# Kernel tuning notes

Measured on AMD Instinct MI355X. Metric: run time of the kernel, lower is better.

Reference implementation:

```python
import jax, jax.numpy as jnp
import numpy as np

BATCH, L = 2, 1024
D_MODEL, D_INNER, D_STATE, DT_RANK, K = 2048, 4096, 16, 128, 4


def setup_inputs() -> dict:
    key = jax.random.key(0)
    ks = jax.random.split(key, 9)
    g = lambda i, shape, s: jax.random.normal(ks[i], shape, jnp.float32) * s
    A_log = jnp.log(jnp.broadcast_to(jnp.arange(1, D_STATE + 1, dtype=jnp.float32),
                                     (D_INNER, D_STATE)))
    return {
        "hidden_states": g(0, (BATCH, L, D_MODEL), 1.0),
        "W_in": g(1, (2 * D_INNER, D_MODEL), 0.02),
        "conv_w": g(2, (D_INNER, K), 0.2),
        "conv_b": g(3, (D_INNER,), 0.02),
        "W_x": g(4, (DT_RANK + 2 * D_STATE, D_INNER), 0.02),
        "W_dt": g(5, (D_INNER, DT_RANK), 0.02),
        "b_dt": g(6, (D_INNER,), 0.02),
        "A_log": A_log,
        "D": jnp.ones((D_INNER,), jnp.float32),
        "W_out": g(7, (D_MODEL, D_INNER), 0.02),
        "b_out": g(8, (D_MODEL,), 0.02),
    }


def reference(hidden_states, W_in, conv_w, conv_b, W_x, W_dt, b_dt, A_log, D, W_out, b_out):
    b, l, _ = hidden_states.shape
    # in_proj -> (b, 2*d_inner, l), split into x and gate z
    xz = jnp.einsum('bld,ed->bel', hidden_states, W_in)
    x, z = jnp.split(xz, 2, axis=1)                      # each (b, d_inner, l)
    # conv_state = F.pad(x, (d_conv - l, 0)): keeps the last d_conv timesteps
    conv_state = x[:, :, -K:]
    # causal depthwise conv1d (left pad K-1) + SiLU
    xc = jax.lax.conv_general_dilated(
        x, conv_w[:, None, :], window_strides=(1,), padding=[(K - 1, 0)],
        feature_group_count=D_INNER, dimension_numbers=('NCH', 'OIH', 'NCH'))
    xc = jax.nn.silu(xc + conv_b[None, :, None])         # (b, d_inner, l)
    # x_proj -> dt / B / C
    x_dbl = jnp.einsum('bdl,ed->ble', xc, W_x)           # (b, l, dt_rank+2n)
    dt, Bm, Cm = jnp.split(x_dbl, [DT_RANK, DT_RANK + D_STATE], axis=-1)
    dt = jnp.einsum('blr,dr->bdl', dt, W_dt)             # (b, d_inner, l), no bias here
    delta = jax.nn.softplus(dt + b_dt[None, :, None])    # dt_proj bias folded into softplus
    A = -jnp.exp(A_log)                                  # (d_inner, d_state)

    def step(state, inp):                                # state: (b, d_inner, d_state)
        d_t, b_t, c_t, u_t = inp                         # (b,d), (b,n), (b,n), (b,d)
        dA = jnp.exp(d_t[..., None] * A)                 # (b, d, n)
        state = dA * state + (d_t * u_t)[..., None] * b_t[:, None, :]
        y_t = jnp.einsum('bdn,bn->bd', state, c_t)
        return state, y_t

    xs = (delta.transpose(2, 0, 1),                      # (l, b, d)
          Bm.transpose(1, 0, 2),                         # (l, b, n)
          Cm.transpose(1, 0, 2),
          xc.transpose(2, 0, 1))
    init = jnp.zeros((b, D_INNER, D_STATE), delta.dtype)
    last_state, ys = jax.lax.scan(step, init, xs)
    y = ys.transpose(1, 2, 0) + D[None, :, None] * xc    # (b, d_inner, l) skip term
    y = y * jax.nn.silu(z)                               # gating
    out = jnp.einsum('bdl,ed->ble', y, W_out) + b_out    # (b, l, d_model)
    return out, conv_state, last_state
```

## Files before the change

kernel.cpp:

```cpp
#include <hip/hip_runtime.h>
#include <stdint.h>
#include <stddef.h>

typedef __bf16 bf16;
typedef __attribute__((ext_vector_type(2))) __bf16 bf16x2;
typedef __attribute__((ext_vector_type(4))) __bf16 bf16x4;
typedef __attribute__((ext_vector_type(8))) __bf16 bf16x8;
typedef __attribute__((ext_vector_type(4))) float floatx4;

#define GAS __attribute__((address_space(1)))
#define LAS __attribute__((address_space(3)))

__device__ __forceinline__ void async16(const void* g, void* l) {
  __builtin_amdgcn_global_load_lds((const GAS void*)g, (LAS void*)l, 16, 0, 0);
}

__device__ __forceinline__ bf16x8 cvt8(const float* p) {
  floatx4 a = *(const floatx4*)p;
  floatx4 b = *(const floatx4*)(p + 4);
  bf16x8 r;
  r[0] = (bf16)a[0]; r[1] = (bf16)a[1]; r[2] = (bf16)a[2]; r[3] = (bf16)a[3];
  r[4] = (bf16)b[0]; r[5] = (bf16)b[1]; r[6] = (bf16)b[2]; r[7] = (bf16)b[3];
  return r;
}

#define ENGINE_BODY(K0_EXPR, NT_EXPR, EPILOGUE)                                \
  __shared__ __attribute__((aligned(16))) bf16 SA[2][2][8192];                 \
  __shared__ __attribute__((aligned(16))) bf16 SB[2][2][8192];                 \
  const int tid = threadIdx.x;                                                 \
  const int wave = tid >> 6;                                                   \
  const int lane = tid & 63;                                                   \
  const int lr = lane & 15;                                                    \
  const int kg = lane >> 4;                                                    \
  const int wm = (wave >> 2) * 128;                                            \
  const int wn = (wave & 3) * 64;                                              \
  const int tilesM = M >> 8;                                                   \
  const int tm = blockIdx.x % tilesM;                                          \
  const int tn = blockIdx.x / tilesM;                                          \
  const int rowBase = tm * 256;                                                \
  const int colBase = tn * 256;                                                \
  const int k0 = (K0_EXPR);                                                    \
  const int NT = (NT_EXPR);                                                    \
  const int srow = tid >> 2;                                                   \
  const int ske = (tid & 3) << 3;                                              \
  const int skel = ske ^ (((srow >> 1) & 3) << 3);                             \
  const size_t aRow0 = (size_t)(rowBase + srow) * lda;                         \
  const size_t aRow1 = aRow0 + (size_t)128 * lda;                              \
  const size_t bRow0 = (size_t)(colBase + srow) * ldb;                         \
  const size_t bRow1 = bRow0 + (size_t)128 * ldb;                              \
  const int keSh = (kg << 3) ^ (((lr >> 1) & 3) << 3);                         \
  floatx4 acc[8][4] = {};                                                      \
  bf16x8 af0[4], af1[4], bgA[4], bgB[4];                                       \
  auto stA = [&](int buf, int kh, int kt) {                                    \
    const int gk = k0 + kt * 64 + kh * 32 + skel;                              \
    bf16* d = &SA[buf][kh][0];                                                 \
    async16(A + aRow0 + gk, d + tid * 8);                                      \
    async16(A + aRow1 + gk, d + 4096 + tid * 8);                               \
  };                                                                           \
  auto stB = [&](int buf, int kh, int kt) {                                    \
    const int gk = k0 + kt * 64 + kh * 32 + skel;                              \
    bf16* d = &SB[buf][kh][0];                                                 \
    async16(B + bRow0 + gk, d + tid * 8);                                      \
    async16(B + bRow1 + gk, d + 4096 + tid * 8);                               \
  };                                                                           \
  stB(0, 0, 0); stA(0, 0, 0); stB(0, 1, 0); stA(0, 1, 0);                      \
  stB(1, 0, 1); stA(1, 0, 1); stB(1, 1, 1);                                    \
  asm volatile("s_waitcnt vmcnt(0)" ::: "memory");                             \
  __builtin_amdgcn_s_barrier();                                                \
  RD_B(bgA, 0, 0);                                                             \
  RD_A(af0, 0, 0, 0);                                                          \
  for (int it = 0; it < (NT >> 1); ++it) {                                     \
    const int T0 = it * 2;                                                     \
    const int T1 = T0 + 1;                                                     \
    const int s1 = (T0 + 2 < NT) ? T0 + 2 : NT - 1;                            \
    const int s2 = (T1 + 2 < NT) ? T1 + 2 : NT - 1;                            \
    PH(RD_A(af1, 0, 0, 1), 4, stA(1, 1, T1), bgA, af0, 0, false)               \
    PH(RD_B(bgB, 0, 1); RD_A(af0, 0, 1, 0), 8, stB(0, 0, s1), bgA, af1, 1,     \
       false)                                                                  \
    PH(RD_A(af1, 0, 1, 1), 4, stA(0, 0, s1), bgB, af0, 0, false)               \
    PH(RD_B(bgA, 1, 0); RD_A(af0, 1, 0, 0), 8, stB(0, 1, s1), bgB, af1, 1,     \
       true)                                                                   \
    PH(RD_A(af1, 1, 0, 1), 4, stA(0, 1, s1), bgA, af0, 0, false)               \
    PH(RD_B(bgB, 1, 1); RD_A(af0, 1, 1, 0), 8, stB(1, 0, s2), bgA, af1, 1,     \
       false)                                                                  \
    PH(RD_A(af1, 1, 1, 1), 4, stA(1, 0, s2), bgB, af0, 0, false)               \
    PH(RD_B(bgA, 0, 0); RD_A(af0, 0, 0, 0), 8, stB(1, 1, s2), bgB, af1, 1,     \
       true)                                                                   \
  }                                                                            \
  asm volatile("s_waitcnt vmcnt(0) lgkmcnt(0)" ::: "memory");                  \
  _Pragma("unroll") for (int m = 0; m < 8; ++m) {                              \
    _Pragma("unroll") for (int n = 0; n < 4; ++n) {                            \
      const int col = colBase + wn + n * 16 + lr;                              \
      _Pragma("unroll") for (int r = 0; r < 4; ++r) {                          \
        const int row = rowBase + wm + m * 16 + kg * 4 + r;                    \
        const size_t idx = (size_t)row * N + col;                              \
        EPILOGUE;                                                              \
      }                                                                        \
    }                                                                          \
  }

#define RD_B(DST, BUF, KH)                                                     \
  _Pragma("unroll") for (int n = 0; n < 4; ++n)                                \
      DST[n] = *(const bf16x8*)&SB[BUF][KH][(wn + n * 16 + lr) * 32 + keSh];
#define RD_A(DST, BUF, KH, MH)                                                 \
  _Pragma("unroll") for (int m = 0; m < 4; ++m)                                \
      DST[m] =                                                                 \
          *(const bf16x8*)&SA[BUF][KH][(wm + ((MH)*4 + m) * 16 + lr) * 32 +    \
                                       keSh];
#define PH(RDS, CNT, STG, BGR, AFR, MH, VM)                                    \
  {                                                                            \
    RDS;                                                                       \
    STG;                                                                       \
    __builtin_amdgcn_s_barrier();                                              \
    asm volatile("s_waitcnt lgkmcnt(" #CNT ")" ::: "memory");                  \
    __builtin_amdgcn_sched_barrier(0);                                         \
    __builtin_amdgcn_s_setprio(1);                                             \
    _Pragma("unroll") for (int m = 0; m < 4; ++m)                              \
      _Pragma("unroll") for (int n = 0; n < 4; ++n)                            \
          acc[(MH)*4 + m][n] = __builtin_amdgcn_mfma_f32_16x16x32_bf16(        \
              AFR[m], BGR[n], acc[(MH)*4 + m][n], 0, 0, 0);                    \
    __builtin_amdgcn_s_setprio(0);                                             \
    __builtin_amdgcn_sched_barrier(0);                                         \
    if constexpr (VM) asm volatile("s_waitcnt vmcnt(2)" ::: "memory");         \
    __builtin_amdgcn_s_barrier();                                              \
  }

__global__ __launch_bounds__(512, 2) void gemm256_8p(
    const bf16* __restrict__ A, const bf16* __restrict__ B,
    bf16* __restrict__ C, int M, int N, int K, int lda, int ldb) {
  ENGINE_BODY(0, K >> 6, C[idx] = (bf16)acc[m][n][r])
}

__global__ __launch_bounds__(512, 2) void gemm256_sk(
    const bf16* __restrict__ A, const bf16* __restrict__ B,
    bf16* __restrict__ C, int M, int N, int K, int lda, int ldb) {
  ENGINE_BODY(blockIdx.y * (K / gridDim.y), (K / gridDim.y) >> 6,
              C[(size_t)blockIdx.y * 4194304 + idx] = (bf16)acc[m][n][r])
}
#undef PH
#undef RD_A
#undef RD_B
#undef ENGINE_BODY

template <int EPI, int AF, int BF, int TM>
__global__ __launch_bounds__(256, 4) void gemm_bt(
    const void* __restrict__ Aptr, const void* __restrict__ Bptr,
    void* __restrict__ Cout, const float* __restrict__ bias,
    int M, int N, int K, int lda, int ldb) {
  __shared__ bf16 As[TM * 32];
  __shared__ bf16 Bs[128 * 32];
  const int tid = threadIdx.x;

  int bx = blockIdx.x, by = blockIdx.y;
  if constexpr (EPI == 6) {
    const int f = blockIdx.x + gridDim.x * blockIdx.y;
    const int gy = gridDim.y >> 3;
    const int i = f >> 3;
    by = (f & 7) * gy + (i % gy);
    bx = i / gy;
  }
  const int rowBase = bx * TM;
  const int colBase = by * 128;
  const int kLen = K / gridDim.z;
  const int k0 = blockIdx.z * kLen;
  const int kIters = kLen / 32;

  const int sRow = tid >> 2;
  const int sCol = (tid & 3) << 3;
  const int wave = tid >> 6;
  const int lane = tid & 63;
  constexpr int MI = 4;
  constexpr int NJ = (TM == 128) ? 4 : 2;
  const int wm = (TM == 128) ? ((wave >> 1) << 6) : 0;
  const int wn = (TM == 128) ? ((wave & 1) << 6) : (wave << 5);
  const int lr = lane & 15;
  const int kg = lane >> 4;

  floatx4 acc[MI][NJ] = {};

  for (int kt = 0; kt < kIters; ++kt) {
    const int kk = k0 + kt * 32;
    __syncthreads();
    if constexpr (AF) {
      const float* pa =
          (const float*)Aptr + (size_t)(rowBase + sRow) * lda + kk + sCol;
      *(bf16x8*)&As[tid * 8] = cvt8(pa);
      if constexpr (TM == 128)
        *(bf16x8*)&As[2048 + tid * 8] = cvt8(pa + (size_t)64 * lda);
    } else {
      const bf16* pa =
          (const bf16*)Aptr + (size_t)(rowBase + sRow) * lda + kk + sCol;
      async16(pa, &As[tid * 8]);
      if constexpr (TM == 128)
        async16(pa + (size_t)64 * lda, &As[2048 + tid * 8]);
    }
    if constexpr (BF) {
      const float* pb =
          (const float*)Bptr + (size_t)(colBase + sRow) * ldb + kk + sCol;
      *(bf16x8*)&Bs[tid * 8] = cvt8(pb);
      *(bf16x8*)&Bs[2048 + tid * 8] = cvt8(pb + (size_t)64 * ldb);
    } else {
      const bf16* pb =
          (const bf16*)Bptr + (size_t)(colBase + sRow) * ldb + kk + sCol;
      async16(pb, &Bs[tid * 8]);
      async16(pb + (size_t)64 * ldb, &Bs[2048 + tid * 8]);
    }
    __syncthreads();

    bf16x8 af[MI], bg[NJ];
#pragma unroll
    for (int i = 0; i < MI; ++i)
      af[i] = *(const bf16x8*)&As[(wm + i * 16 + lr) * 32 + kg * 8];
#pragma unroll
    for (int j = 0; j < NJ; ++j)
      bg[j] = *(const bf16x8*)&Bs[(wn + j * 16 + lr) * 32 + kg * 8];
#pragma unroll
    for (int i = 0; i < MI; ++i)
#pragma unroll
      for (int j = 0; j < NJ; ++j)
        acc[i][j] = __builtin_amdgcn_mfma_f32_16x16x32_bf16(af[i], bg[j],
                                                            acc[i][j], 0, 0, 0);
  }

#pragma unroll
  for (int i = 0; i < MI; ++i) {
#pragma unroll
    for (int j = 0; j < NJ; ++j) {
      const int col = colBase + wn + j * 16 + lr;
      float bv = 0.f;
      if constexpr (EPI == 2 || EPI == 3) bv = bias[col];
#pragma unroll
      for (int r = 0; r < 4; ++r) {
        const int row = rowBase + wm + i * 16 + kg * 4 + r;
        const size_t idx = (size_t)row * N + col;
        float v = acc[i][j][r];
        if constexpr (EPI == 0) {
          ((bf16*)Cout)[idx] = (bf16)v;
        } else if constexpr (EPI == 1) {
          atomicAdd((float*)Cout + idx, v);
        } else if constexpr (EPI == 2) {
          v += bv;
          const float t = __expf(v);
          const float sp = (v > 20.f) ? v : __logf(1.f + t);
          ((bf16*)Cout)[idx] = (bf16)sp;
        } else if constexpr (EPI == 3) {
          ((float*)Cout)[idx] = v + bv;
        } else if constexpr (EPI == 4) {
          ((float*)Cout)[(size_t)blockIdx.z * 524288 + idx] = v;
        } else {
          ((bf16*)Cout)[(size_t)blockIdx.z * 4194304 + idx] = (bf16)v;
        }
      }
    }
  }
}

__global__ __launch_bounds__(256) void reduce_xdbl(
    const float* __restrict__ part, float* __restrict__ xdbl,
    bf16* __restrict__ xdblb) {
  const size_t i4 = ((size_t)blockIdx.x * 256 + threadIdx.x) * 4;
  floatx4 s = {};
#pragma unroll
  for (int z = 0; z < 8; ++z) {
    const floatx4 v = *(const floatx4*)&part[(size_t)z * 524288 + i4];
    s[0] += v[0]; s[1] += v[1]; s[2] += v[2]; s[3] += v[3];
  }
  *(floatx4*)&xdbl[i4] = s;
  const int col = (int)(i4 & 255);
  if (col < 128) {
    const size_t row = i4 >> 8;
    bf16x4 b;
    b[0] = (bf16)s[0]; b[1] = (bf16)s[1]; b[2] = (bf16)s[2]; b[3] = (bf16)s[3];
    *(bf16x4*)&xdblb[row * 128 + col] = b;
  }
}

__global__ __launch_bounds__(256) void reduce_out4(
    const bf16* __restrict__ part, const float* __restrict__ bias,
    float* __restrict__ outp) {
  const size_t i4 = ((size_t)blockIdx.x * 256 + threadIdx.x) * 4;
  floatx4 s = *(const floatx4*)&bias[i4 & 2047];
#pragma unroll
  for (int z = 0; z < 4; ++z) {
    const bf16x4 v = *(const bf16x4*)&part[(size_t)z * 4194304 + i4];
    s[0] += (float)v[0]; s[1] += (float)v[1];
    s[2] += (float)v[2]; s[3] += (float)v[3];
  }
  *(floatx4*)&outp[i4] = s;
}

#define PC0 524288UL
#define PC1 2621440UL
#define PC2 2686976UL
#define PC3 3735552UL
#define PC4 3866624UL
__global__ __launch_bounds__(256) void prep_all(
    const float* __restrict__ h, const float* __restrict__ wi,
    const float* __restrict__ wd, const float* __restrict__ wo,
    const float* __restrict__ wx, bf16* __restrict__ hb,
    bf16* __restrict__ wib, bf16* __restrict__ wdb, bf16* __restrict__ wob,
    bf16* __restrict__ wxp) {
  const size_t c = (size_t)blockIdx.x * 256 + threadIdx.x;
  if (c < PC0) {
    const size_t e = c * 8;
    *(bf16x8*)&hb[e] = cvt8(&h[e]);
  } else if (c < PC1) {
    const size_t e = (c - PC0) * 8;
    *(bf16x8*)&wib[e] = cvt8(&wi[e]);
  } else if (c < PC2) {
    const size_t e = (c - PC1) * 8;
    *(bf16x8*)&wdb[e] = cvt8(&wd[e]);
  } else if (c < PC3) {
    const size_t e = (c - PC2) * 8;
    *(bf16x8*)&wob[e] = cvt8(&wo[e]);
  } else if (c < PC4) {
    const size_t e = (c - PC3) * 8;
    if ((e >> 12) < 160) {
      *(bf16x8*)&wxp[e] = cvt8(&wx[e]);
    } else {
      bf16x8 z = {};
      *(bf16x8*)&wxp[e] = z;
    }
  }
}

__global__ void wxpad_prep(const float* __restrict__ Wx,
                           bf16* __restrict__ WXPAD) {
  const int idx = blockIdx.x * 256 + threadIdx.x;
  const int row = idx >> 12;
  WXPAD[idx] = (row < 160) ? (bf16)Wx[idx] : (bf16)0.f;
}

__global__ __launch_bounds__(256) void conv_v8(
    const bf16* __restrict__ XZ, const float* __restrict__ conv_w,
    const float* __restrict__ conv_b, bf16* __restrict__ XC,
    float* __restrict__ outConv) {
  const int idx = blockIdx.x * 256 + threadIdx.x;
  const int d8 = (idx & 511) << 3;
  const int row = idx >> 9;
  const int l = row & 1023;
  float acc[8];
  {
    const floatx4 cb0 = *(const floatx4*)&conv_b[d8];
    const floatx4 cb1 = *(const floatx4*)&conv_b[d8 + 4];
#pragma unroll
    for (int j = 0; j < 4; ++j) { acc[j] = cb0[j]; acc[4 + j] = cb1[j]; }
  }
  float w[8][4];
#pragma unroll
  for (int j = 0; j < 8; ++j) {
    const floatx4 cw = *(const floatx4*)&conv_w[(d8 + j) * 4];
#pragma unroll
    for (int k = 0; k < 4; ++k) w[j][k] = cw[k];
  }
  if (l >= 3) {
#pragma unroll
    for (int k = 0; k < 4; ++k) {
      const bf16x8 x = *(const bf16x8*)&XZ[(size_t)(row - 3 + k) * 8192 + d8];
#pragma unroll
      for (int j = 0; j < 8; ++j) acc[j] += w[j][k] * (float)x[j];
    }
  } else {
#pragma unroll
    for (int k = 0; k < 4; ++k) {
      if (l - 3 + k >= 0) {
        const bf16x8 x = *(const bf16x8*)&XZ[(size_t)(row - 3 + k) * 8192 + d8];
#pragma unroll
        for (int j = 0; j < 8; ++j) acc[j] += w[j][k] * (float)x[j];
      }
    }
  }
  bf16x8 o;
#pragma unroll
  for (int j = 0; j < 8; ++j)
    o[j] = (bf16)(acc[j] / (1.f + __expf(-acc[j])));
  *(bf16x8*)&XC[(size_t)row * 4096 + d8] = o;
  if (idx < 4096) {
#pragma unroll
    for (int j = 0; j < 8; ++j) {
      const int e = idx * 8 + j;
      const int k = e & 3;
      const int dd = (e >> 2) & 4095;
      const int b = e >> 14;
      outConv[e] = (float)XZ[(size_t)(b * 1024 + 1020 + k) * 8192 + dd];
    }
  }
}

#define NCH 32
#define CLEN 32
#define LOG2E 1.44269504088896f

__global__ __launch_bounds__(256) void scan_phase1(
    const bf16* __restrict__ DELTA, const bf16* __restrict__ XC,
    const float* __restrict__ XDBL, const float* __restrict__ A_log,
    bf16* __restrict__ P, bf16* __restrict__ Lc) {
  const int pd = blockIdx.x * 256 + threadIdx.x;
  const int c = blockIdx.y;
  const int b = pd >> 11;
  const int d = (pd & 2047) << 1;
  const int bd = (b << 12) + d;
  float A2[32], st[32], p[32];
#pragma unroll
  for (int n = 0; n < 32; ++n) {
    A2[n] = -__expf(A_log[d * 16 + n]) * LOG2E;
    st[n] = 0.f;
    p[n] = 1.f;
  }
  size_t row = (size_t)b * 1024 + (size_t)c * CLEN;
  for (int t = 0; t < CLEN; ++t, ++row) {
    const bf16x2 d2 = *(const bf16x2*)&DELTA[row * 4096 + d];
    const bf16x2 u2 = *(const bf16x2*)&XC[row * 4096 + d];
    const float dlt0 = (float)d2[0], dlt1 = (float)d2[1];
    const float du0 = dlt0 * (float)u2[0], du1 = dlt1 * (float)u2[1];
    const float* __restrict__ Bp = XDBL + row * 256 + 128;
#pragma unroll
    for (int n = 0; n < 16; ++n) {
      const float Bv = Bp[n];
      const float dA0 = exp2f(dlt0 * A2[n]);
      st[n] = dA0 * st[n] + du0 * Bv;
      p[n] *= dA0;
      const float dA1 = exp2f(dlt1 * A2[16 + n]);
      st[16 + n] = dA1 * st[16 + n] + du1 * Bv;
      p[16 + n] *= dA1;
    }
  }
  const size_t o = ((size_t)c * 8192 + bd) * 16;
  bf16x8 pk[4], lk[4];
#pragma unroll
  for (int n = 0; n < 32; ++n) {
    pk[n >> 3][n & 7] = (bf16)p[n];
    lk[n >> 3][n & 7] = (bf16)st[n];
  }
#pragma unroll
  for (int q = 0; q < 4; ++q) {
    *(bf16x8*)&P[o + q * 8] = pk[q];
    *(bf16x8*)&Lc[o + q * 8] = lk[q];
  }
}

__global__ __launch_bounds__(64) void scan_phase2(
    const bf16* __restrict__ P, const bf16* __restrict__ Lc,
    bf16* __restrict__ In, float* __restrict__ lastOut) {
  const int bd = blockIdx.x * 64 + threadIdx.x;
  float st[16] = {};
  for (int c = 0; c < NCH; ++c) {
    const size_t o = ((size_t)c * 8192 + bd) * 16;
    const bf16x8 p0 = *(const bf16x8*)&P[o];
    const bf16x8 p1 = *(const bf16x8*)&P[o + 8];
    const bf16x8 l0 = *(const bf16x8*)&Lc[o];
    const bf16x8 l1 = *(const bf16x8*)&Lc[o + 8];
    bf16x8 w0, w1;
#pragma unroll
    for (int n = 0; n < 8; ++n) {
      w0[n] = (bf16)st[n];
      w1[n] = (bf16)st[8 + n];
    }
    *(bf16x8*)&In[o] = w0;
    *(bf16x8*)&In[o + 8] = w1;
#pragma unroll
    for (int n = 0; n < 8; ++n) {
      st[n] = (float)p0[n] * st[n] + (float)l0[n];
      st[8 + n] = (float)p1[n] * st[8 + n] + (float)l1[n];
    }
  }
  const int b = bd >> 12;
  const int d = bd & 4095;
#pragma unroll
  for (int n = 0; n < 16; ++n)
    lastOut[(size_t)b * 65536 + d * 16 + n] = st[n];
}

__global__ __launch_bounds__(256) void scan_phase3(
    const bf16* __restrict__ DELTA, const bf16* __restrict__ XC,
    const bf16* __restrict__ XZ, const float* __restrict__ XDBL,
    const float* __restrict__ A_log, const float* __restrict__ Dp,
    const bf16* __restrict__ In, bf16* __restrict__ Y) {
  const int pd = blockIdx.x * 256 + threadIdx.x;
  const int c = blockIdx.y;
  const int b = pd >> 11;
  const int d = (pd & 2047) << 1;
  const int bd = (b << 12) + d;
  float A2[32], st[32];
  const size_t o = ((size_t)c * 8192 + bd) * 16;
#pragma unroll
  for (int q = 0; q < 4; ++q) {
    const bf16x8 v = *(const bf16x8*)&In[o + q * 8];
#pragma unroll
    for (int j = 0; j < 8; ++j) st[q * 8 + j] = (float)v[j];
  }
#pragma unroll
  for (int n = 0; n < 32; ++n)
    A2[n] = -__expf(A_log[d * 16 + n]) * LOG2E;
  const float Dd0 = Dp[d], Dd1 = Dp[d + 1];
  size_t row = (size_t)b * 1024 + (size_t)c * CLEN;
  for (int t = 0; t < CLEN; ++t, ++row) {
    const bf16x2 d2 = *(const bf16x2*)&DELTA[row * 4096 + d];
    const bf16x2 u2 = *(const bf16x2*)&XC[row * 4096 + d];
    const bf16x2 z2 = *(const bf16x2*)&XZ[row * 8192 + 4096 + d];
    const float dlt0 = (float)d2[0], dlt1 = (float)d2[1];
    const float u0 = (float)u2[0], u1 = (float)u2[1];
    const float du0 = dlt0 * u0, du1 = dlt1 * u1;
    const float* __restrict__ Bp = XDBL + row * 256 + 128;
    float y0 = 0.f, y1 = 0.f;
#pragma unroll
    for (int n = 0; n < 16; ++n) {
      const float Bv = Bp[n];
      const float Cv = Bp[16 + n];
      const float dA0 = exp2f(dlt0 * A2[n]);
      st[n] = dA0 * st[n] + du0 * Bv;
      y0 += st[n] * Cv;
      const float dA1 = exp2f(dlt1 * A2[16 + n]);
      st[16 + n] = dA1 * st[16 + n] + du1 * Bv;
      y1 += st[16 + n] * Cv;
    }
    const float z0 = (float)z2[0], z1 = (float)z2[1];
    const float sig0 = 1.f / (1.f + __expf(-z0));
    const float sig1 = 1.f / (1.f + __expf(-z1));
    bf16x2 yo;
    yo[0] = (bf16)((y0 + Dd0 * u0) * (z0 * sig0));
    yo[1] = (bf16)((y1 + Dd1 * u1) * (z1 * sig1));
    *(bf16x2*)&Y[row * 4096 + d] = yo;
  }
}

#define OFF_XZ 0UL
#define OFF_XC 33554432UL
#define OFF_DELTA 50331648UL
#define OFF_Y 83886080UL
#define OFF_XDBL 100663296UL
#define OFF_WXPAD 103284736UL
#define OFF_P 105381888UL
#define OFF_L 113770496UL
#define OFF_HBF 122159104UL
#define OFF_WINBF 130547712UL
#define OFF_WDTBF 164102144UL
#define OFF_WOUTBF 165150720UL
#define WS_NEED_CAST 181927936UL

extern "C" void kernel_launch(void* const* d_in, const int* in_sizes, int n_in,
                              void* d_out, int out_size, void* d_ws,
                              size_t ws_size, hipStream_t stream) {
  const float* hidden = (const float*)d_in[0];
  const float* W_in = (const float*)d_in[1];
  const float* conv_w = (const float*)d_in[2];
  const float* conv_b = (const float*)d_in[3];
  const float* W_x = (const float*)d_in[4];
  const float* W_dt = (const float*)d_in[5];
  const float* b_dt = (const float*)d_in[6];
  const float* A_log = (const float*)d_in[7];
  const float* Dvec = (const float*)d_in[8];
  const float* W_out = (const float*)d_in[9];
  const float* b_out = (const float*)d_in[10];

  char* ws = (char*)d_ws;
  bf16* XZ = (bf16*)(ws + OFF_XZ);
  bf16* XC = (bf16*)(ws + OFF_XC);
  bf16* DELTA = (bf16*)(ws + OFF_DELTA);
  float* PART = (float*)(ws + OFF_DELTA + 16777216UL);
  bf16* SLAB3 = (bf16*)(ws + OFF_XZ);
  bf16* Y = (bf16*)(ws + OFF_Y);
  float* XDBL = (float*)(ws + OFF_XDBL);
  bf16* XDBLB = (bf16*)(ws + OFF_HBF);
  bf16* WXPAD = (bf16*)(ws + OFF_WXPAD);
  bf16* P = (bf16*)(ws + OFF_P);
  bf16* Lc = (bf16*)(ws + OFF_L);

  float* out = (float*)d_out;
  float* out_conv = out + 4194304;
  float* out_last = out + 4227072;
  bf16* In = (bf16*)out;

  const bool castOK = ws_size >= WS_NEED_CAST;
  if (castOK) {
    bf16* HBF = (bf16*)(ws + OFF_HBF);
    bf16* WINBF = (bf16*)(ws + OFF_WINBF);
    bf16* WDTBF = (bf16*)(ws + OFF_WDTBF);
    bf16* WOUTBF = (bf16*)(ws + OFF_WOUTBF);
    prep_all<<<15104, 256, 0, stream>>>(hidden, W_in, W_dt, W_out, W_x, HBF,
                                        WINBF, WDTBF, WOUTBF, WXPAD);
    gemm256_8p<<<dim3(256), 512, 0, stream>>>(HBF, WINBF, XZ, 2048, 8192,
                                              2048, 2048, 2048);
    conv_v8<<<4096, 256, 0, stream>>>(XZ, conv_w, conv_b, XC, out_conv);
    gemm_bt<4, 0, 0, 64><<<dim3(32, 2, 8), 256, 0, stream>>>(
        XC, WXPAD, PART, nullptr, 2048, 256, 4096, 4096, 4096);
    reduce_xdbl<<<512, 256, 0, stream>>>(PART, XDBL, XDBLB);
    gemm_bt<2, 0, 0, 64><<<dim3(32, 32, 1), 256, 0, stream>>>(
        XDBLB, WDTBF, DELTA, b_dt, 2048, 4096, 128, 128, 128);
    scan_phase1<<<dim3(16, NCH), 256, 0, stream>>>(DELTA, XC, XDBL, A_log, P,
                                                   Lc);
    scan_phase2<<<128, 64, 0, stream>>>(P, Lc, In, out_last);
    scan_phase3<<<dim3(16, NCH), 256, 0, stream>>>(DELTA, XC, XZ, XDBL, A_log,
                                                   Dvec, In, Y);
    gemm256_sk<<<dim3(64, 4), 512, 0, stream>>>(Y, WOUTBF, SLAB3, 2048, 2048,
                                                4096, 4096, 4096);
    reduce_out4<<<4096, 256, 0, stream>>>(SLAB3, b_out, out);
  } else {
    wxpad_prep<<<4096, 256, 0, stream>>>(W_x, WXPAD);
    gemm_bt<0, 1, 1, 128><<<dim3(16, 64, 1), 256, 0, stream>>>(
        hidden, W_in, XZ, nullptr, 2048, 8192, 2048, 2048, 2048);
    conv_v8<<<4096, 256, 0, stream>>>(XZ, conv_w, conv_b, XC, out_conv);
    gemm_bt<4, 0, 0, 64><<<dim3(32, 2, 8), 256, 0, stream>>>(
        XC, WXPAD, PART, nullptr, 2048, 256, 4096, 4096, 4096);
    reduce_xdbl<<<512, 256, 0, stream>>>(PART, XDBL, XDBLB);
    gemm_bt<2, 1, 1, 64><<<dim3(32, 32, 1), 256, 0, stream>>>(
        XDBL, W_dt, DELTA, b_dt, 2048, 4096, 128, 256, 128);
    scan_phase1<<<dim3(16, NCH), 256, 0, stream>>>(DELTA, XC, XDBL, A_log, P,
                                                   Lc);
    scan_phase2<<<128, 64, 0, stream>>>(P, Lc, In, out_last);
    scan_phase3<<<dim3(16, NCH), 256, 0, stream>>>(DELTA, XC, XZ, XDBL, A_log,
                                                   Dvec, In, Y);
    gemm_bt<6, 0, 1, 128><<<dim3(16, 16, 4), 256, 0, stream>>>(
        Y, W_out, SLAB3, nullptr, 2048, 2048, 4096, 4096, 4096);
    reduce_out4<<<4096, 256, 0, stream>>>(SLAB3, b_out, out);
  }
}
```

Measured before the change: 443.5 us.

## Fuse three scan phases into one cooperative kernel with grid syncs

Replaces the three separate chunked-scan launches (chunk-local scan, cross-chunk carry propagation, final recompute with output gating) with a single cooperative kernel that uses grid-wide syncs between phases. The goal is to remove two kernel launch boundaries and to keep the A coefficients in registers across phases. In exchange, the grid is fixed at 256 blocks of 512 threads with launch_bounds forcing one block per CU. Phase 2 runs on only 128 blocks of 64 threads while the rest of the grid idles at the barrier. If the cooperative launch fails, the code falls back to the original three kernels.

```diff
diff --git a/kernel.cpp b/kernel.cpp
--- a/kernel.cpp
+++ b/kernel.cpp
@@ -1,6 +1,9 @@
 #include <hip/hip_runtime.h>
+#include <hip/hip_cooperative_groups.h>
 #include <stdint.h>
 #include <stddef.h>
+
+namespace cg = cooperative_groups;
 
 typedef __bf16 bf16;
 typedef __attribute__((ext_vector_type(2))) __bf16 bf16x2;
@@ -524,6 +527,139 @@
   }
 }
 
+__global__ __launch_bounds__(512, 1) void scan_fused(
+    const bf16* __restrict__ DELTA, const bf16* __restrict__ XC,
+    const bf16* __restrict__ XZ, const float* __restrict__ XDBL,
+    const float* __restrict__ A_log, const float* __restrict__ Dp,
+    bf16* __restrict__ P, bf16* __restrict__ Lc, bf16* __restrict__ In,
+    float* __restrict__ lastOut, bf16* __restrict__ Y) {
+  cg::grid_group grid = cg::this_grid();
+  const int blk = blockIdx.x;
+  const int tid = threadIdx.x;
+  const int pd = (blk & 7) * 512 + tid;
+  const int c = blk >> 3;
+  const int b = pd >> 11;
+  const int d = (pd & 2047) << 1;
+  const int bd = (b << 12) + d;
+  const size_t o = ((size_t)c * 8192 + bd) * 16;
+
+  float A2[32];
+#pragma unroll
+  for (int n = 0; n < 32; ++n)
+    A2[n] = -__expf(A_log[d * 16 + n]) * LOG2E;
+
+  {
+    float st[32], p[32];
+#pragma unroll
+    for (int n = 0; n < 32; ++n) { st[n] = 0.f; p[n] = 1.f; }
+    size_t row = (size_t)b * 1024 + (size_t)c * CLEN;
+    for (int t = 0; t < CLEN; ++t, ++row) {
+      const bf16x2 d2 = *(const bf16x2*)&DELTA[row * 4096 + d];
+      const bf16x2 u2 = *(const bf16x2*)&XC[row * 4096 + d];
+      const float dlt0 = (float)d2[0], dlt1 = (float)d2[1];
+      const float du0 = dlt0 * (float)u2[0], du1 = dlt1 * (float)u2[1];
+      const float* __restrict__ Bp = XDBL + row * 256 + 128;
+#pragma unroll
+      for (int n = 0; n < 16; ++n) {
+        const float Bv = Bp[n];
+        const float dA0 = exp2f(dlt0 * A2[n]);
+        st[n] = dA0 * st[n] + du0 * Bv;
+        p[n] *= dA0;
+        const float dA1 = exp2f(dlt1 * A2[16 + n]);
+        st[16 + n] = dA1 * st[16 + n] + du1 * Bv;
+        p[16 + n] *= dA1;
+      }
+    }
+    bf16x8 pk[4], lk[4];
+#pragma unroll
+    for (int n = 0; n < 32; ++n) {
+      pk[n >> 3][n & 7] = (bf16)p[n];
+      lk[n >> 3][n & 7] = (bf16)st[n];
+    }
+#pragma unroll
+    for (int q = 0; q < 4; ++q) {
+      *(bf16x8*)&P[o + q * 8] = pk[q];
+      *(bf16x8*)&Lc[o + q * 8] = lk[q];
+    }
+  }
+  __threadfence();
+  grid.sync();
+  __threadfence();
+
+  if (blk < 128 && tid < 64) {
+    const int bd2 = blk * 64 + tid;
+    float st[16] = {};
+    for (int cc = 0; cc < NCH; ++cc) {
+      const size_t o2 = ((size_t)cc * 8192 + bd2) * 16;
+      const bf16x8 p0 = *(const bf16x8*)&P[o2];
+      const bf16x8 p1 = *(const bf16x8*)&P[o2 + 8];
+      const bf16x8 l0 = *(const bf16x8*)&Lc[o2];
+      const bf16x8 l1 = *(const bf16x8*)&Lc[o2 + 8];
+      bf16x8 w0, w1;
+#pragma unroll
+      for (int n = 0; n < 8; ++n) {
+        w0[n] = (bf16)st[n];
+        w1[n] = (bf16)st[8 + n];
+      }
+      *(bf16x8*)&In[o2] = w0;
+      *(bf16x8*)&In[o2 + 8] = w1;
+#pragma unroll
+      for (int n = 0; n < 8; ++n) {
+        st[n] = (float)p0[n] * st[n] + (float)l0[n];
+        st[8 + n] = (float)p1[n] * st[8 + n] + (float)l1[n];
+      }
+    }
+    const int b2 = bd2 >> 12;
+    const int d2i = bd2 & 4095;
+#pragma unroll
+    for (int n = 0; n < 16; ++n)
+      lastOut[(size_t)b2 * 65536 + d2i * 16 + n] = st[n];
+  }
+  __threadfence();
+  grid.sync();
+  __threadfence();
+
+  {
+    float st[32];
+#pragma unroll
+    for (int q = 0; q < 4; ++q) {
+      const bf16x8 v = *(const bf16x8*)&In[o + q * 8];
+#pragma unroll
+      for (int j = 0; j < 8; ++j) st[q * 8 + j] = (float)v[j];
+    }
+    const float Dd0 = Dp[d], Dd1 = Dp[d + 1];
+    size_t row = (size_t)b * 1024 + (size_t)c * CLEN;
+    for (int t = 0; t < CLEN; ++t, ++row) {
+      const bf16x2 d2 = *(const bf16x2*)&DELTA[row * 4096 + d];
+      const bf16x2 u2 = *(const bf16x2*)&XC[row * 4096 + d];
+      const bf16x2 z2 = *(const bf16x2*)&XZ[row * 8192 + 4096 + d];
+      const float dlt0 = (float)d2[0], dlt1 = (float)d2[1];
+      const float u0 = (float)u2[0], u1 = (float)u2[1];
+      const float du0 = dlt0 * u0, du1 = dlt1 * u1;
+      const float* __restrict__ Bp = XDBL + row * 256 + 128;
+      float y0 = 0.f, y1 = 0.f;
+#pragma unroll
+      for (int n = 0; n < 16; ++n) {
+        const float Bv = Bp[n];
+        const float Cv = Bp[16 + n];
+        const float dA0 = exp2f(dlt0 * A2[n]);
+        st[n] = dA0 * st[n] + du0 * Bv;
+        y0 += st[n] * Cv;
+        const float dA1 = exp2f(dlt1 * A2[16 + n]);
+        st[16 + n] = dA1 * st[16 + n] + du1 * Bv;
+        y1 += st[16 + n] * Cv;
+      }
+      const float z0 = (float)z2[0], z1 = (float)z2[1];
+      const float sig0 = 1.f / (1.f + __expf(-z0));
+      const float sig1 = 1.f / (1.f + __expf(-z1));
+      bf16x2 yo;
+      yo[0] = (bf16)((y0 + Dd0 * u0) * (z0 * sig0));
+      yo[1] = (bf16)((y1 + Dd1 * u1) * (z1 * sig1));
+      *(bf16x2*)&Y[row * 4096 + d] = yo;
+    }
+  }
+}
+
 #define OFF_XZ 0UL
 #define OFF_XC 33554432UL
 #define OFF_DELTA 50331648UL
@@ -587,11 +723,23 @@
     reduce_xdbl<<<512, 256, 0, stream>>>(PART, XDBL, XDBLB);
     gemm_bt<2, 0, 0, 64><<<dim3(32, 32, 1), 256, 0, stream>>>(
         XDBLB, WDTBF, DELTA, b_dt, 2048, 4096, 128, 128, 128);
-    scan_phase1<<<dim3(16, NCH), 256, 0, stream>>>(DELTA, XC, XDBL, A_log, P,
-                                                   Lc);
-    scan_phase2<<<128, 64, 0, stream>>>(P, Lc, In, out_last);
-    scan_phase3<<<dim3(16, NCH), 256, 0, stream>>>(DELTA, XC, XZ, XDBL, A_log,
-                                                   Dvec, In, Y);
+    {
+      const bf16* dA = DELTA; const bf16* xcA = XC; const bf16* xzA = XZ;
+      const float* xdA = XDBL; const float* alA = A_log; const float* dpA = Dvec;
+      bf16* pA = P; bf16* lA = Lc; bf16* inA = In; float* loA = out_last;
+      bf16* yA = Y;
+      void* sargs[] = {(void*)&dA, (void*)&xcA, (void*)&xzA, (void*)&xdA,
+                       (void*)&alA, (void*)&dpA, (void*)&pA, (void*)&lA,
+                       (void*)&inA, (void*)&loA, (void*)&yA};
+      if (hipLaunchCooperativeKernel((void*)scan_fused, dim3(256), dim3(512),
+                                     sargs, 0, stream) != hipSuccess) {
+        scan_phase1<<<dim3(16, NCH), 256, 0, stream>>>(DELTA, XC, XDBL, A_log,
+                                                       P, Lc);
+        scan_phase2<<<128, 64, 0, stream>>>(P, Lc, In, out_last);
+        scan_phase3<<<dim3(16, NCH), 256, 0, stream>>>(DELTA, XC, XZ, XDBL,
+                                                       A_log, Dvec, In, Y);
+      }
+    }
     gemm256_sk<<<dim3(64, 4), 512, 0, stream>>>(Y, WOUTBF, SLAB3, 2048, 2048,
                                                 4096, 4096, 4096);
     reduce_out4<<<4096, 256, 0, stream>>>(SLAB3, b_out, out);
```

Measured after the change: 720.5 us. 62.5% more time.
